# Kernel tuning notes

Hardware: AMD Instinct MI355X
Metric: run time of the kernel (lower is better)

Reference implementation:

```python
import jax, jax.numpy as jnp
import numpy as np

GROUPSIZE = 128
ZERO_POINT = 8  # (maxq + 1) // 2 with maxq = 2**4 - 1


def setup_inputs() -> dict:
    key = jax.random.key(0)
    kA, ks, kq = jax.random.split(key, 3)
    M, K, N = 4096, 4096, 4096
    A = jax.random.normal(kA, (M, K), dtype=jnp.float32)
    # per-group scales, positive and small like real quantization scales
    s = jax.random.uniform(ks, (K // GROUPSIZE, N), dtype=jnp.float32) * 0.02 + 1e-3
    # int4 weights in [0, 15], packed 8 nibbles per int32 word along n
    nib = jax.random.randint(kq, (K, N), 0, 16, dtype=jnp.int32).astype(jnp.uint32)
    shifts = (4 * jnp.arange(8, dtype=jnp.uint32))
    q_u = (nib.reshape(K, N // 8, 8) << shifts).sum(axis=-1)  # uint32 (K, N//8)
    q = jax.lax.bitcast_convert_type(q_u, jnp.int32)
    return {"A": A, "s": s, "q": q}


def reference(A, s, q):
    # Unpack 8 int4 nibbles per int32 word: (K, N//8) -> (K, N)
    shifts = 4 * jnp.arange(8, dtype=jnp.int32)
    nib = (q[:, :, None] >> shifts) & 0xF  # (K, N//8, 8)
    nib = nib.reshape(q.shape[0], -1)      # (K, N)
    # Symmetric dequant with zero-point 8 and per-group (groupsize=128 rows) scales
    w = (nib.astype(A.dtype) - ZERO_POINT) * jnp.repeat(s.astype(A.dtype), GROUPSIZE, axis=0)
    return A @ w  # (M, N)
```

## Files before the change

kernel.cpp:

```cpp
#include <hip/hip_runtime.h>
#include <stdint.h>

#define GM 4096
#define GN 4096
#define GK 4096
#define QW (GN/8)

typedef __attribute__((ext_vector_type(4))) int   i32x4;
typedef __attribute__((ext_vector_type(8))) short bf16x8;
typedef __attribute__((ext_vector_type(4))) float f32x4;

#define AS1 __attribute__((address_space(1)))
#define AS3 __attribute__((address_space(3)))

static __device__ __forceinline__ void glds16(const void* g, void* l) {
  __builtin_amdgcn_global_load_lds((const AS1 uint32_t*)g, (AS3 uint32_t*)l, 16, 0, 0);
}

static __device__ __forceinline__ uint32_t bf16pack_rn(float hi, float lo) {
  uint32_t h = __float_as_uint(hi) + 0x8000u;
  uint32_t l = __float_as_uint(lo) + 0x8000u;
  return __builtin_amdgcn_perm(h, l, 0x07060302u);
}

static __device__ __forceinline__ uint32_t pack4i8(int b0, int b1, int b2, int b3) {
  return ((uint32_t)b0 & 255u) | (((uint32_t)b1 & 255u) << 8) |
         (((uint32_t)b2 & 255u) << 16) | (((uint32_t)b3 & 255u) << 24);
}

__global__ void __launch_bounds__(256) prep(const float* __restrict__ A,
                                            const float* __restrict__ S,
                                            const uint32_t* __restrict__ Q,
                                            int8_t* __restrict__ Ai,
                                            float* __restrict__ ascale,
                                            int8_t* __restrict__ Wt,
                                            float* __restrict__ wscale) {
  __shared__ uint32_t T32[128 * 32];
  __shared__ float4   red[8][32];
  __shared__ float    winv_l[128];

  const int b   = blockIdx.x;
  const int tid = threadIdx.x;

  if (b < 1024) {
    const int lane = tid & 63;
    const int row  = b * 4 + (tid >> 6);
    const float* src = A + (size_t)row * GK;
    float4 v[16];
    float m = 0.f;
    #pragma unroll
    for (int i = 0; i < 16; ++i) {
      v[i] = *(const float4*)(src + i * 256 + lane * 4);
      m = fmaxf(m, fmaxf(fmaxf(fabsf(v[i].x), fabsf(v[i].y)),
                         fmaxf(fabsf(v[i].z), fabsf(v[i].w))));
    }
    #pragma unroll
    for (int off = 32; off >= 1; off >>= 1)
      m = fmaxf(m, __shfl_xor(m, off, 64));
    const float rmax = fmaxf(m, 1e-20f);
    const float inv  = 127.0f / rmax;
    #pragma unroll
    for (int i = 0; i < 16; ++i) {
      uint32_t bb = pack4i8((int)__builtin_rintf(v[i].x * inv),
                            (int)__builtin_rintf(v[i].y * inv),
                            (int)__builtin_rintf(v[i].z * inv),
                            (int)__builtin_rintf(v[i].w * inv));
      *(uint32_t*)(Ai + (size_t)row * GK + i * 256 + lane * 4) = bb;
    }
    if (lane == 0) ascale[row] = rmax * (1.0f / 127.0f);
  } else if (b < 2048) {
    const int wb = b - 1024;
    const int n0 = (wb & 31) * 128;
    const int k0 = (wb >> 5) * 128;
    const int g  = wb >> 5;
    const int w  = tid & 15;
    const int kb = tid >> 4;

    {
      const int c4 = tid & 31;
      const int g8 = tid >> 5;
      float4 m4 = make_float4(0.f, 0.f, 0.f, 0.f);
      #pragma unroll
      for (int gg = 0; gg < 4; ++gg) {
        float4 sv = *(const float4*)(S + (size_t)(g8 * 4 + gg) * GN + n0 + c4 * 4);
        m4.x = fmaxf(m4.x, sv.x); m4.y = fmaxf(m4.y, sv.y);
        m4.z = fmaxf(m4.z, sv.z); m4.w = fmaxf(m4.w, sv.w);
      }
      red[g8][c4] = m4;
      __syncthreads();
      if (g8 == 0) {
        float4 m = red[0][c4];
        #pragma unroll
        for (int rr = 1; rr < 8; ++rr) {
          float4 o = red[rr][c4];
          m.x = fmaxf(m.x, o.x); m.y = fmaxf(m.y, o.y);
          m.z = fmaxf(m.z, o.z); m.w = fmaxf(m.w, o.w);
        }
        winv_l[c4 * 4 + 0] = 127.0f / (8.0f * m.x);
        winv_l[c4 * 4 + 1] = 127.0f / (8.0f * m.y);
        winv_l[c4 * 4 + 2] = 127.0f / (8.0f * m.z);
        winv_l[c4 * 4 + 3] = 127.0f / (8.0f * m.w);
      }
      __syncthreads();
    }

    float r[8], c[8];
    {
      const float* sp = S + (size_t)g * GN + n0 + w * 8;
      float4 sa = *(const float4*)sp, sb = *(const float4*)(sp + 4);
      float4 ia = *(const float4*)&winv_l[w * 8];
      float4 ib = *(const float4*)&winv_l[w * 8 + 4];
      const float sv[8] = {sa.x, sa.y, sa.z, sa.w, sb.x, sb.y, sb.z, sb.w};
      const float iv[8] = {ia.x, ia.y, ia.z, ia.w, ib.x, ib.y, ib.z, ib.w};
      #pragma unroll
      for (int j = 0; j < 8; ++j) { r[j] = sv[j] * iv[j]; c[j] = -8.0f * r[j]; }
    }

    const int swz = 4 * (w & 7);
    #pragma unroll
    for (int c2 = 0; c2 < 2; ++c2) {
      uint32_t q[4];
      #pragma unroll
      for (int i = 0; i < 4; ++i)
        q[i] = Q[(size_t)(k0 + c2 * 64 + kb * 4 + i) * QW + (n0 >> 3) + w];
      const int kword = c2 * 16 + kb;
      #pragma unroll
      for (int j = 0; j < 8; ++j) {
        int bb[4];
        #pragma unroll
        for (int i = 0; i < 4; ++i) {
          float nib = (float)((q[i] >> (4 * j)) & 0xFu);
          bb[i] = (int)__builtin_rintf(fmaf(nib, r[j], c[j]));
        }
        T32[(w * 8 + j) * 32 + (kword ^ swz)] = pack4i8(bb[0], bb[1], bb[2], bb[3]);
      }
    }
    __syncthreads();
    #pragma unroll
    for (int p = 0; p < 4; ++p) {
      int idx = p * 256 + tid;
      int n = idx >> 3, gr = idx & 7;
      uint4 v = *(const uint4*)(&T32[n * 32 + (gr ^ ((n >> 3) & 7)) * 4]);
      *(uint4*)(Wt + (size_t)(n0 + n) * GK + k0 + gr * 16) = v;
    }
  } else {
    const int n = (b - 2048) * 256 + tid;
    float m = 0.f;
    #pragma unroll 8
    for (int gg = 0; gg < 32; ++gg) m = fmaxf(m, S[(size_t)gg * GN + n]);
    wscale[n] = m * (8.0f / 127.0f);
  }
}

__global__ void __launch_bounds__(512, 2) gemm_i8(const int8_t* __restrict__ Ai,
                                                  const int8_t* __restrict__ Wi,
                                                  const float* __restrict__ ascale,
                                                  const float* __restrict__ wscale,
                                                  float* __restrict__ C) {
  __shared__ __align__(16) int8_t As[2][256 * 128];
  __shared__ __align__(16) int8_t Bs[2][256 * 128];

  const int tid = threadIdx.x;
  const int bid = blockIdx.y * gridDim.x + blockIdx.x;
  const int swb = ((bid & 7) << 5) | (bid >> 3);
  const int m0  = (swb >> 4) * 256;
  const int n0  = (swb & 15) * 256;

  const int lane = tid & 63;
  const int wid  = tid >> 6;
  const int wm   = wid >> 2;
  const int wn   = wid & 3;
  const int col  = lane & 15;
  const int quad = lane >> 4;
  const int sw   = col & 7;

  const int ur0   = tid >> 3;
  const int pc    = tid & 7;
  const int qo    = ((pc ^ (ur0 & 7)) << 4);
  const int arow0 = ur0;
  const int brow0 = (ur0 & 31) + ((ur0 & 32) << 1);
  const size_t aoff = (size_t)(m0 + arow0) * GK + qo;
  const size_t boff = (size_t)(n0 + brow0) * GK + qo;
  const int dA0 = arow0 * 128 + pc * 16;
  const int dB0 = brow0 * 128 + pc * 16;

#define STAGE_A(b, kt, hi) do {                                              \
    const int8_t* s_ = Ai + aoff + (size_t)(hi) * 64 * GK + (size_t)(kt) * 128; \
    glds16(s_,                   &As[b][dA0 + (hi) * 8192]);                 \
    glds16(s_ + (size_t)128 * GK, &As[b][dA0 + (hi) * 8192 + 16384]);        \
  } while (0)
#define STAGE_B(b, kt, hi) do {                                              \
    const int8_t* s_ = Wi + boff + (size_t)(hi) * 32 * GK + (size_t)(kt) * 128; \
    glds16(s_,                   &Bs[b][dB0 + (hi) * 4096]);                 \
    glds16(s_ + (size_t)128 * GK, &Bs[b][dB0 + (hi) * 4096 + 16384]);        \
  } while (0)

  const int cq0 = ((quad    ) ^ sw) << 4;
  const int cq1 = ((quad + 4) ^ sw) << 4;
  const int aRd = (wm * 128 + col) * 128;
  const int bRd = (wn * 64  + col) * 128;

  i32x4 af[4][2], bf0[2][2], bf1[2][2];
  i32x4 acc[8][4];
  #pragma unroll
  for (int i = 0; i < 8; ++i)
    #pragma unroll
    for (int j = 0; j < 4; ++j)
      acc[i][j] = (i32x4){0, 0, 0, 0};

#define LDA_(b, h) do {                                                      \
    _Pragma("unroll")                                                        \
    for (int m_ = 0; m_ < 4; ++m_) {                                         \
      af[m_][0] = *(const i32x4*)(&As[b][aRd + (h) * 8192 + m_ * 2048 + cq0]); \
      af[m_][1] = *(const i32x4*)(&As[b][aRd + (h) * 8192 + m_ * 2048 + cq1]); \
    }                                                                        \
  } while (0)
#define LDB_(b, g, BF) do {                                                  \
    _Pragma("unroll")                                                        \
    for (int n_ = 0; n_ < 2; ++n_) {                                         \
      BF[n_][0] = *(const i32x4*)(&Bs[b][bRd + (g) * 4096 + n_ * 2048 + cq0]); \
      BF[n_][1] = *(const i32x4*)(&Bs[b][bRd + (g) * 4096 + n_ * 2048 + cq1]); \
    }                                                                        \
  } while (0)
#define MFMAQ_(h, g, BF) do {                                                \
    _Pragma("unroll")                                                        \
    for (int m_ = 0; m_ < 4; ++m_)                                           \
      _Pragma("unroll")                                                      \
      for (int n_ = 0; n_ < 2; ++n_) {                                       \
        acc[(h)*4+m_][(g)*2+n_] = __builtin_amdgcn_mfma_i32_16x16x64_i8(     \
            af[m_][0], BF[n_][0], acc[(h)*4+m_][(g)*2+n_], 0, 0, 0);         \
        acc[(h)*4+m_][(g)*2+n_] = __builtin_amdgcn_mfma_i32_16x16x64_i8(     \
            af[m_][1], BF[n_][1], acc[(h)*4+m_][(g)*2+n_], 0, 0, 0);         \
      }                                                                      \
  } while (0)
#define BAR()   __builtin_amdgcn_s_barrier()
#define VM6()   asm volatile("s_waitcnt vmcnt(6)" ::: "memory")
#define PRIO1() __builtin_amdgcn_s_setprio(1)
#define PRIO0() __builtin_amdgcn_s_setprio(0)

  STAGE_A(0, 0, 0); STAGE_A(0, 0, 1); STAGE_B(0, 0, 0); STAGE_B(0, 0, 1);
  STAGE_A(1, 1, 0); STAGE_B(1, 1, 0); STAGE_B(1, 1, 1);
  VM6();
  BAR();

  for (int it = 0; it < GK / 256; ++it) {
    const int t1 = 2 * it + 1;
    const int t2 = (2 * it + 2) & 31;
    const int t3 = (2 * it + 3) & 31;

    STAGE_A(1, t1, 1);
    LDA_(0, 0); LDB_(0, 0, bf0);
    PRIO1(); MFMAQ_(0, 0, bf0); PRIO0();
    BAR();
    STAGE_A(0, t2, 0);
    LDB_(0, 1, bf1);
    PRIO1(); MFMAQ_(0, 1, bf1); PRIO0();
    BAR();
    STAGE_B(0, t2, 0);
    LDA_(0, 1);
    PRIO1(); MFMAQ_(1, 1, bf1); PRIO0();
    BAR();
    STAGE_B(0, t2, 1);
    PRIO1(); MFMAQ_(1, 0, bf0); PRIO0();
    VM6();
    BAR();
    STAGE_A(0, t2, 1);
    LDA_(1, 0); LDB_(1, 0, bf0);
    PRIO1(); MFMAQ_(0, 0, bf0); PRIO0();
    BAR();
    STAGE_A(1, t3, 0);
    LDB_(1, 1, bf1);
    PRIO1(); MFMAQ_(0, 1, bf1); PRIO0();
    BAR();
    STAGE_B(1, t3, 0);
    LDA_(1, 1);
    PRIO1(); MFMAQ_(1, 1, bf1); PRIO0();
    BAR();
    STAGE_B(1, t3, 1);
    PRIO1(); MFMAQ_(1, 0, bf0); PRIO0();
    VM6();
    BAR();
  }

  #pragma unroll
  for (int h = 0; h < 2; ++h)
    #pragma unroll
    for (int m = 0; m < 4; ++m) {
      const int rbase = m0 + wm * 128 + h * 64 + m * 16 + quad * 4;
      float4 a4 = *(const float4*)(ascale + rbase);
      const float ar[4] = {a4.x, a4.y, a4.z, a4.w};
      #pragma unroll
      for (int g = 0; g < 2; ++g)
        #pragma unroll
        for (int n = 0; n < 2; ++n) {
          const int cbase = n0 + wn * 64 + g * 32 + n * 16 + col;
          const float ws = wscale[cbase];
          #pragma unroll
          for (int r = 0; r < 4; ++r)
            C[(size_t)(rbase + r) * GN + cbase]
              = (float)acc[h * 4 + m][g * 2 + n][r] * (ar[r] * ws);
        }
    }
#undef STAGE_A
#undef STAGE_B
#undef LDA_
#undef LDB_
#undef MFMAQ_
#undef BAR
#undef VM6
#undef PRIO1
#undef PRIO0
}

#define BM 128
#define BN 128
#define BK 32

__global__ void __launch_bounds__(256) w4a32_gemm(
    const float* __restrict__ A,
    const float* __restrict__ S,
    const uint32_t* __restrict__ Q,
    float* __restrict__ C)
{
  __shared__ __align__(16) ushort As[BM*BK];
  __shared__ __align__(16) ushort Bs[BN*BK];

  const int tid  = threadIdx.x;
  const int m0   = blockIdx.y*BM;
  const int n0   = blockIdx.x*BN;
  const int wcol  = tid & 15;
  const int kpair = tid >> 4;
  const int ln   = tid & 63;
  const int wid  = tid >> 6;
  const int wm   = (wid >> 1) * 64;
  const int wn   = (wid & 1) * 64;
  const int col  = ln & 15;
  const int quad = ln >> 4;

  f32x4 acc[4][4];
  #pragma unroll
  for (int i=0;i<4;++i)
    #pragma unroll
    for (int j=0;j<4;++j)
      acc[i][j] = (f32x4){0.f,0.f,0.f,0.f};

  float sv[8], cv[8];
  float4 spf0, spf1;

  const float*    Abase = A + (size_t)m0 * GK;
  const uint32_t* Qbase = Q + (size_t)(n0>>3) + wcol;

  {
    const float* sp = S + n0 + wcol*8;
    spf0 = *(const float4*)sp;
    spf1 = *(const float4*)(sp + 4);
  }

  float4 a4[4];
  uint32_t wqa, wqb;
  #pragma unroll
  for (int i=0;i<4;++i) {
    int f = tid + i*256;
    a4[i] = *(const float4*)(Abase + (size_t)(f>>3)*GK + ((f&7)*4));
  }
  wqa = Qbase[(size_t)(2*kpair)   * QW];
  wqb = Qbase[(size_t)(2*kpair+1) * QW];

  for (int k0 = 0; k0 < GK; k0 += BK) {
    if ((k0 & 127) == 0) {
      sv[0]=spf0.x; sv[1]=spf0.y; sv[2]=spf0.z; sv[3]=spf0.w;
      sv[4]=spf1.x; sv[5]=spf1.y; sv[6]=spf1.z; sv[7]=spf1.w;
      #pragma unroll
      for (int j=0;j<8;++j) cv[j] = -8.0f * sv[j];
    }

    #pragma unroll
    for (int i=0;i<4;++i) {
      int f = tid + i*256;
      int row = f>>3, c4 = f&7;
      *(uint2*)(&As[row*BK + c4*4]) =
        make_uint2(bf16pack_rn(a4[i].y, a4[i].x), bf16pack_rn(a4[i].w, a4[i].z));
    }

    {
      const int kk = (2*kpair) ^ (8*(wcol&3));
      #pragma unroll
      for (int j=0;j<8;++j) {
        float fa = (float)((wqa >> (4*j)) & 0xFu);
        float fb = (float)((wqb >> (4*j)) & 0xFu);
        float wa = fmaf(fa, sv[j], cv[j]);
        float wb = fmaf(fb, sv[j], cv[j]);
        int n = wcol*8 + j;
        *(uint32_t*)(&Bs[n*BK + kk]) = bf16pack_rn(wb, wa);
      }
    }

    int kn = k0 + BK; if (kn >= GK) kn = 0;
    if ((kn & 127) == 0) {
      const float* sp = S + (size_t)(kn>>7)*GN + n0 + wcol*8;
      spf0 = *(const float4*)sp;
      spf1 = *(const float4*)(sp + 4);
    }
    #pragma unroll
    for (int i=0;i<4;++i) {
      int f = tid + i*256;
      a4[i] = *(const float4*)(Abase + (size_t)(f>>3)*GK + kn + ((f&7)*4));
    }
    wqa = Qbase[(size_t)(kn + 2*kpair)   * QW];
    wqb = Qbase[(size_t)(kn + 2*kpair+1) * QW];

    __syncthreads();

    bf16x8 af[4], bfr[4];
    #pragma unroll
    for (int t=0;t<4;++t) {
      af[t] = *(const bf16x8*)(&As[(wm + t*16 + col)*BK + quad*8]);
      int n = wn + t*16 + col;
      int kk = (quad*8) ^ (8*((n>>3)&3));
      bfr[t] = *(const bf16x8*)(&Bs[n*BK + kk]);
    }
    #pragma unroll
    for (int mt=0;mt<4;++mt)
      #pragma unroll
      for (int nt=0;nt<4;++nt)
        acc[mt][nt] = __builtin_amdgcn_mfma_f32_16x16x32_bf16(
                          af[mt], bfr[nt], acc[mt][nt], 0, 0, 0);

    __syncthreads();
  }

  #pragma unroll
  for (int mt=0;mt<4;++mt)
    #pragma unroll
    for (int nt=0;nt<4;++nt)
      #pragma unroll
      for (int r=0;r<4;++r)
        C[(size_t)(m0 + wm + mt*16 + quad*4 + r)*GN + n0 + wn + nt*16 + col]
          = acc[mt][nt][r];
}

extern "C" void kernel_launch(void* const* d_in, const int* in_sizes, int n_in,
                              void* d_out, int out_size, void* d_ws, size_t ws_size,
                              hipStream_t stream) {
  const float*    A = (const float*)d_in[0];
  const float*    S = (const float*)d_in[1];
  const uint32_t* Q = (const uint32_t*)d_in[2];
  float*          C = (float*)d_out;

  const size_t need = (size_t)GM * GK + (size_t)GN * GK + 3 * 4096 * 4 + 4096;
  if (ws_size >= need) {
    int8_t* Ai  = (int8_t*)d_ws;
    int8_t* Wt  = Ai + (size_t)GM * GK;
    float* ascale = (float*)(Wt + (size_t)GN * GK);
    float* wscale = ascale + 4096;
    prep<<<dim3(1024 + 1024 + 16), dim3(256), 0, stream>>>(A, S, Q, Ai, ascale, Wt, wscale);
    gemm_i8<<<dim3(GN / 256, GM / 256), dim3(512), 0, stream>>>(Ai, Wt, ascale, wscale, C);
  } else {
    w4a32_gemm<<<dim3(GN / BN, GM / BM), dim3(256), 0, stream>>>(A, S, Q, C);
  }
}
```

Before: 183.8 us.

## Shrink int8 GEMM tile to 128x256 with triple-buffered K=64 pipeline

```diff
diff --git a/kernel.cpp b/kernel.cpp
--- a/kernel.cpp
+++ b/kernel.cpp
@@ -152,18 +152,18 @@
   }
 }
 
-__global__ void __launch_bounds__(512, 2) gemm_i8(const int8_t* __restrict__ Ai,
+__global__ void __launch_bounds__(512, 4) gemm_i8(const int8_t* __restrict__ Ai,
                                                   const int8_t* __restrict__ Wi,
                                                   const float* __restrict__ ascale,
                                                   const float* __restrict__ wscale,
                                                   float* __restrict__ C) {
-  __shared__ __align__(16) int8_t As[2][256 * 128];
-  __shared__ __align__(16) int8_t Bs[2][256 * 128];
+  __shared__ __align__(16) int8_t As[3][128 * 64];
+  __shared__ __align__(16) int8_t Bs[3][256 * 64];
 
   const int tid = threadIdx.x;
   const int bid = blockIdx.y * gridDim.x + blockIdx.x;
-  const int swb = ((bid & 7) << 5) | (bid >> 3);
-  const int m0  = (swb >> 4) * 256;
+  const int swb = ((bid & 7) << 6) | (bid >> 3);
+  const int m0  = (swb >> 4) * 128;
   const int n0  = (swb & 15) * 256;
 
   const int lane = tid & 63;
@@ -172,144 +172,96 @@
   const int wn   = wid & 3;
   const int col  = lane & 15;
   const int quad = lane >> 4;
-  const int sw   = col & 7;
-
-  const int ur0   = tid >> 3;
-  const int pc    = tid & 7;
-  const int qo    = ((pc ^ (ur0 & 7)) << 4);
-  const int arow0 = ur0;
-  const int brow0 = (ur0 & 31) + ((ur0 & 32) << 1);
-  const size_t aoff = (size_t)(m0 + arow0) * GK + qo;
-  const size_t boff = (size_t)(n0 + brow0) * GK + qo;
-  const int dA0 = arow0 * 128 + pc * 16;
-  const int dB0 = brow0 * 128 + pc * 16;
-
-#define STAGE_A(b, kt, hi) do {                                              \
-    const int8_t* s_ = Ai + aoff + (size_t)(hi) * 64 * GK + (size_t)(kt) * 128; \
-    glds16(s_,                   &As[b][dA0 + (hi) * 8192]);                 \
-    glds16(s_ + (size_t)128 * GK, &As[b][dA0 + (hi) * 8192 + 16384]);        \
+
+  const int srow = tid >> 2;
+  const int qo   = ((tid & 3) ^ (srow & 3)) << 4;
+  const int8_t* Asrc  = Ai + (size_t)(m0 + srow) * GK + qo;
+  const int8_t* Bsrc  = Wi + (size_t)(n0 + srow) * GK + qo;
+  const int8_t* Bsrc2 = Bsrc + (size_t)128 * GK;
+
+#define STAGE(b, ko) do {                                    \
+    glds16(Asrc  + (ko), &As[b][tid * 16]);                  \
+    glds16(Bsrc  + (ko), &Bs[b][tid * 16]);                  \
+    glds16(Bsrc2 + (ko), &Bs[b][8192 + tid * 16]);           \
   } while (0)
-#define STAGE_B(b, kt, hi) do {                                              \
-    const int8_t* s_ = Wi + boff + (size_t)(hi) * 32 * GK + (size_t)(kt) * 128; \
-    glds16(s_,                   &Bs[b][dB0 + (hi) * 4096]);                 \
-    glds16(s_ + (size_t)128 * GK, &Bs[b][dB0 + (hi) * 4096 + 16384]);        \
-  } while (0)
-
-  const int cq0 = ((quad    ) ^ sw) << 4;
-  const int cq1 = ((quad + 4) ^ sw) << 4;
-  const int aRd = (wm * 128 + col) * 128;
-  const int bRd = (wn * 64  + col) * 128;
-
-  i32x4 af[4][2], bf0[2][2], bf1[2][2];
-  i32x4 acc[8][4];
+
+  const int cq  = ((quad ^ (col & 3)) << 4);
+  const int aRd = (wm * 64 + col) * 64 + cq;
+  const int bRd = (wn * 64 + col) * 64 + cq;
+
+  i32x4 af[4], bf[4];
+  i32x4 acc[4][4];
   #pragma unroll
-  for (int i = 0; i < 8; ++i)
+  for (int i = 0; i < 4; ++i)
     #pragma unroll
     for (int j = 0; j < 4; ++j)
       acc[i][j] = (i32x4){0, 0, 0, 0};
 
-#define LDA_(b, h) do {                                                      \
-    _Pragma("unroll")                                                        \
-    for (int m_ = 0; m_ < 4; ++m_) {                                         \
-      af[m_][0] = *(const i32x4*)(&As[b][aRd + (h) * 8192 + m_ * 2048 + cq0]); \
-      af[m_][1] = *(const i32x4*)(&As[b][aRd + (h) * 8192 + m_ * 2048 + cq1]); \
-    }                                                                        \
+#define LD_(b) do {                                                   \
+    _Pragma("unroll")                                                 \
+    for (int x_ = 0; x_ < 4; ++x_) {                                  \
+      af[x_] = *(const i32x4*)(&As[b][aRd + x_ * 1024]);              \
+      bf[x_] = *(const i32x4*)(&Bs[b][bRd + x_ * 1024]);              \
+    }                                                                 \
   } while (0)
-#define LDB_(b, g, BF) do {                                                  \
-    _Pragma("unroll")                                                        \
-    for (int n_ = 0; n_ < 2; ++n_) {                                         \
-      BF[n_][0] = *(const i32x4*)(&Bs[b][bRd + (g) * 4096 + n_ * 2048 + cq0]); \
-      BF[n_][1] = *(const i32x4*)(&Bs[b][bRd + (g) * 4096 + n_ * 2048 + cq1]); \
-    }                                                                        \
+#define MFMA16_() do {                                                \
+    _Pragma("unroll")                                                 \
+    for (int m_ = 0; m_ < 4; ++m_)                                    \
+      _Pragma("unroll")                                               \
+      for (int n_ = 0; n_ < 4; ++n_)                                  \
+        acc[m_][n_] = __builtin_amdgcn_mfma_i32_16x16x64_i8(          \
+            af[m_], bf[n_], acc[m_][n_], 0, 0, 0);                    \
   } while (0)
-#define MFMAQ_(h, g, BF) do {                                                \
-    _Pragma("unroll")                                                        \
-    for (int m_ = 0; m_ < 4; ++m_)                                           \
-      _Pragma("unroll")                                                      \
-      for (int n_ = 0; n_ < 2; ++n_) {                                       \
-        acc[(h)*4+m_][(g)*2+n_] = __builtin_amdgcn_mfma_i32_16x16x64_i8(     \
-            af[m_][0], BF[n_][0], acc[(h)*4+m_][(g)*2+n_], 0, 0, 0);         \
-        acc[(h)*4+m_][(g)*2+n_] = __builtin_amdgcn_mfma_i32_16x16x64_i8(     \
-            af[m_][1], BF[n_][1], acc[(h)*4+m_][(g)*2+n_], 0, 0, 0);         \
-      }                                                                      \
-  } while (0)
-#define BAR()   __builtin_amdgcn_s_barrier()
-#define VM6()   asm volatile("s_waitcnt vmcnt(6)" ::: "memory")
+#define VM3()   asm volatile("s_waitcnt vmcnt(3)" ::: "memory")
+#define BARM()  asm volatile("s_barrier" ::: "memory")
 #define PRIO1() __builtin_amdgcn_s_setprio(1)
 #define PRIO0() __builtin_amdgcn_s_setprio(0)
 
-  STAGE_A(0, 0, 0); STAGE_A(0, 0, 1); STAGE_B(0, 0, 0); STAGE_B(0, 0, 1);
-  STAGE_A(1, 1, 0); STAGE_B(1, 1, 0); STAGE_B(1, 1, 1);
-  VM6();
-  BAR();
-
-  for (int it = 0; it < GK / 256; ++it) {
-    const int t1 = 2 * it + 1;
-    const int t2 = (2 * it + 2) & 31;
-    const int t3 = (2 * it + 3) & 31;
-
-    STAGE_A(1, t1, 1);
-    LDA_(0, 0); LDB_(0, 0, bf0);
-    PRIO1(); MFMAQ_(0, 0, bf0); PRIO0();
-    BAR();
-    STAGE_A(0, t2, 0);
-    LDB_(0, 1, bf1);
-    PRIO1(); MFMAQ_(0, 1, bf1); PRIO0();
-    BAR();
-    STAGE_B(0, t2, 0);
-    LDA_(0, 1);
-    PRIO1(); MFMAQ_(1, 1, bf1); PRIO0();
-    BAR();
-    STAGE_B(0, t2, 1);
-    PRIO1(); MFMAQ_(1, 0, bf0); PRIO0();
-    VM6();
-    BAR();
-    STAGE_A(0, t2, 1);
-    LDA_(1, 0); LDB_(1, 0, bf0);
-    PRIO1(); MFMAQ_(0, 0, bf0); PRIO0();
-    BAR();
-    STAGE_A(1, t3, 0);
-    LDB_(1, 1, bf1);
-    PRIO1(); MFMAQ_(0, 1, bf1); PRIO0();
-    BAR();
-    STAGE_B(1, t3, 0);
-    LDA_(1, 1);
-    PRIO1(); MFMAQ_(1, 1, bf1); PRIO0();
-    BAR();
-    STAGE_B(1, t3, 1);
-    PRIO1(); MFMAQ_(1, 0, bf0); PRIO0();
-    VM6();
-    BAR();
-  }
+#define STEP(B_CUR, B_NXT, KO_NXT) do {                               \
+    VM3();                               \
+    BARM();                            \
+    STAGE(B_NXT, (KO_NXT));       \
+    LD_(B_CUR);                                                       \
+    PRIO1(); MFMA16_(); PRIO0();                                      \
+  } while (0)
+
+  STAGE(0, 0);
+  STAGE(1, 64);
+
+  for (int it = 0; it < 21; ++it) {
+    const int t = 3 * it;
+    STEP(0, 2, ((t + 2) & 63) << 6);
+    STEP(1, 0, ((t + 3) & 63) << 6);
+    STEP(2, 1, ((t + 4) & 63) << 6);
+  }
+  VM3();
+  BARM();
+  LD_(0);
+  PRIO1(); MFMA16_(); PRIO0();
 
   #pragma unroll
-  for (int h = 0; h < 2; ++h)
-    #pragma unroll
-    for (int m = 0; m < 4; ++m) {
-      const int rbase = m0 + wm * 128 + h * 64 + m * 16 + quad * 4;
-      float4 a4 = *(const float4*)(ascale + rbase);
-      const float ar[4] = {a4.x, a4.y, a4.z, a4.w};
-      #pragma unroll
-      for (int g = 0; g < 2; ++g)
-        #pragma unroll
-        for (int n = 0; n < 2; ++n) {
-          const int cbase = n0 + wn * 64 + g * 32 + n * 16 + col;
-          const float ws = wscale[cbase];
-          #pragma unroll
-          for (int r = 0; r < 4; ++r)
-            C[(size_t)(rbase + r) * GN + cbase]
-              = (float)acc[h * 4 + m][g * 2 + n][r] * (ar[r] * ws);
-        }
-    }
-#undef STAGE_A
-#undef STAGE_B
-#undef LDA_
-#undef LDB_
-#undef MFMAQ_
-#undef BAR
-#undef VM6
+  for (int mt = 0; mt < 4; ++mt) {
+    const int rbase = m0 + wm * 64 + mt * 16 + quad * 4;
+    float4 a4 = *(const float4*)(ascale + rbase);
+    const float ar[4] = {a4.x, a4.y, a4.z, a4.w};
+    #pragma unroll
+    for (int nt = 0; nt < 4; ++nt) {
+      const int cbase = n0 + wn * 64 + nt * 16 + col;
+      const float ws = wscale[cbase];
+      #pragma unroll
+      for (int r = 0; r < 4; ++r)
+        C[(size_t)(rbase + r) * GN + cbase]
+          = (float)acc[mt][nt][r] * (ar[r] * ws);
+    }
+  }
+#undef STAGE
+#undef LD_
+#undef MFMA16_
+#undef VM3
+#undef BARM
 #undef PRIO1
 #undef PRIO0
+#undef STEP
 }
 
 #define BM 128
@@ -454,7 +406,7 @@
     float* ascale = (float*)(Wt + (size_t)GN * GK);
     float* wscale = ascale + 4096;
     prep<<<dim3(1024 + 1024 + 16), dim3(256), 0, stream>>>(A, S, Q, Ai, ascale, Wt, wscale);
-    gemm_i8<<<dim3(GN / 256, GM / 256), dim3(512), 0, stream>>>(Ai, Wt, ascale, wscale, C);
+    gemm_i8<<<dim3(16, 32), dim3(512), 0, stream>>>(Ai, Wt, ascale, wscale, C);
   } else {
     w4a32_gemm<<<dim3(GN / BN, GM / BM), dim3(256), 0, stream>>>(A, S, Q, C);
   }
```

New measurement: 192.5 us. +4.7%, slower.
